# Kernel tuning notes

Hardware: AMD Instinct MI355X
Metric: run time of the kernel (lower is better)

## Reference

```python
import jax, jax.numpy as jnp
import numpy as np

B, S, D, H = 4, 1024, 256, 8  # batch, seq, d_model (== head_dim), n_heads
SCALE = 1.0 / float(np.sqrt(D))  # source references undefined self.scale; use 1/sqrt(d_model)


def setup_inputs() -> dict:
    key = jax.random.key(0)
    ks = jax.random.split(key, 11)
    w = 0.02
    return {
        "value_input": jax.random.normal(ks[0], (B, S, D), dtype=jnp.float32),
        "key_input": jax.random.normal(ks[1], (B, S, D), dtype=jnp.float32),
        "query_input": jax.random.normal(ks[2], (B, S, D), dtype=jnp.float32),
        "Wv": jax.random.normal(ks[3], (D, D * H), dtype=jnp.float32) * w,
        "bv": jnp.zeros((D * H,), dtype=jnp.float32),
        "Wk": jax.random.normal(ks[4], (D, D * H), dtype=jnp.float32) * w,
        "bk": jnp.zeros((D * H,), dtype=jnp.float32),
        "Wq": jax.random.normal(ks[5], (D, D * H), dtype=jnp.float32) * w,
        "bq": jnp.zeros((D * H,), dtype=jnp.float32),
        "Wo": jax.random.normal(ks[6], (D * H, D), dtype=jnp.float32) * w,
        "bo": jnp.zeros((D,), dtype=jnp.float32),
    }


def reference(value_input, key_input, query_input, Wv, bv, Wk, bk, Wq, bq, Wo, bo):
    # Fused QKV-style projections, then split into heads along last dim.
    # torch.split(..., d_model, dim=-1) == reshape to (B, S, H, D).
    v = (value_input @ Wv + bv).reshape(B, S, H, D)
    k = (key_input @ Wk + bk).reshape(B, S, H, D)
    q = (query_input @ Wq + bq).reshape(B, S, H, D)
    # Source: dot = k @ q^T  -> scores[b,h,key_pos,query_pos]
    scores = jnp.einsum('bkhd,bqhd->bhkq', k, q) * SCALE
    # Softmax over dim=-1 == the QUERY axis (faithful to source, nonstandard).
    attn = jax.nn.softmax(scores, axis=-1)
    # attn @ v : contract query axis with v's seq axis -> output indexed by key pos
    out_h = jnp.einsum('bhkq,bqhd->bkhd', attn, v)
    concat = out_h.reshape(B, S, H * D)
    return concat @ Wo + bo
```

## Files before the change

### kernel.cpp

```cpp
#include <hip/hip_runtime.h>
#include <cstddef>
#include <cstdint>

#define Bz 4
#define Sz 1024
#define Dm 256
#define Hh 8
#define DHh 2048
#define SCALE 0.0625f

typedef __attribute__((ext_vector_type(8))) short short8;
typedef __attribute__((ext_vector_type(16))) float f32x16;

__device__ inline unsigned short f2bf(float f){
  unsigned u = __float_as_uint(f);
  u += 0x7FFFu + ((u >> 16) & 1u);
  return (unsigned short)(u >> 16);
}
__device__ inline unsigned pk2(float a, float b){
  return (unsigned)f2bf(a) | ((unsigned)f2bf(b) << 16);
}
__device__ inline void gll16(const void* g, void* l){
  __builtin_amdgcn_global_load_lds((const __attribute__((address_space(1))) unsigned*)g,
                                   (__attribute__((address_space(3))) unsigned*)l, 16, 0, 0);
}
__device__ inline short8 lds8(const char* p){ return *(const short8*)p; }
__device__ inline f32x16 MM(short8 a, short8 b, f32x16 c){
  return __builtin_amdgcn_mfma_f32_32x32x16_bf16(a, b, c, 0, 0, 0);
}
__device__ inline f32x16 z16(){ f32x16 v;
#pragma unroll
  for(int i=0;i<16;i++) v[i]=0.f; return v; }

__global__ __launch_bounds__(256) void cvt_all(
    const float* __restrict__ S0, const float* __restrict__ S1, const float* __restrict__ S2,
    unsigned short* __restrict__ D0, unsigned short* __restrict__ D1, unsigned short* __restrict__ D2,
    const float* __restrict__ W0, const float* __restrict__ W1,
    const float* __restrict__ W2, const float* __restrict__ W3,
    unsigned short* __restrict__ T0, unsigned short* __restrict__ T1,
    unsigned short* __restrict__ T2, unsigned short* __restrict__ T3){
  __shared__ float t[32][33];
  int bx = blockIdx.x;
  if(bx < 3072){
    const int seg = bx >> 10;
    const float* src = seg==0 ? S0 : seg==1 ? S1 : S2;
    unsigned short* dst = seg==0 ? D0 : seg==1 ? D1 : D2;
    const int i = (bx & 1023)*256 + threadIdx.x;
    float4 v = ((const float4*)src)[i];
    ushort4 o; o.x=f2bf(v.x); o.y=f2bf(v.y); o.z=f2bf(v.z); o.w=f2bf(v.w);
    ((ushort4*)dst)[i] = o;
    return;
  }
  bx -= 3072;
  const int z = bx >> 9, inner = bx & 511;
  const float* W = z==0 ? W0 : z==1 ? W1 : z==2 ? W2 : W3;
  unsigned short* T = z==0 ? T0 : z==1 ? T1 : z==2 ? T2 : T3;
  const int K = (z<3) ? 256 : 2048;
  const int N = (z<3) ? 2048 : 256;
  const int n0 = (z<3) ? (inner & 63)*32 : (inner & 7)*32;
  const int k0 = (z<3) ? (inner >> 6)*32 : (inner >> 3)*32;
  const int a = threadIdx.x >> 5, c = threadIdx.x & 31;
#pragma unroll
  for(int p=0;p<4;p++)
    t[a + p*8][c] = W[(size_t)(k0 + a + p*8)*N + n0 + c];
  __syncthreads();
#pragma unroll
  for(int p=0;p<4;p++)
    T[(size_t)(n0 + a + p*8)*K + k0 + c] = f2bf(t[c][a + p*8]);
}

__global__ __launch_bounds__(256) void gemm_proj_all(
    const unsigned short* __restrict__ A0, const unsigned short* __restrict__ A1,
    const unsigned short* __restrict__ A2,
    const unsigned short* __restrict__ B0, const unsigned short* __restrict__ B1,
    const unsigned short* __restrict__ B2,
    const float* __restrict__ bias0, const float* __restrict__ bias1,
    const float* __restrict__ bias2,
    unsigned short* __restrict__ C0, unsigned short* __restrict__ C1,
    unsigned short* __restrict__ C2){
  __shared__ __align__(16) char sm[65536];
  const int z = blockIdx.z;
  const unsigned short* A = z==0 ? A0 : z==1 ? A1 : A2;
  const unsigned short* Bt = z==0 ? B0 : z==1 ? B1 : B2;
  const float* bias = z==0 ? bias0 : z==1 ? bias1 : bias2;
  unsigned short* C = z==0 ? C0 : z==1 ? C1 : C2;
  const int tid = threadIdx.x, w = tid>>6, lane = tid&63, l31 = lane&31, hp = lane>>5;
  const int wm = (w>>1)*64, wn = (w&1)*64;
  const int bm = blockIdx.y*128, bn = blockIdx.x*128;
  f32x16 acc[2][2]; acc[0][0]=z16(); acc[0][1]=z16(); acc[1][0]=z16(); acc[1][1]=z16();

  auto STAGE = [&](int db, int kk){
#pragma unroll
    for(int j=0;j<4;j++){
      int ci = (w*4+j)*64 + lane;
      int m = ci>>3, sl = ci&7;
      gll16(A  + (size_t)(bm+m)*256 + kk + ((sl ^ (m&7))<<3), sm + db*32768 + (w*4+j)*1024);
      gll16(Bt + (size_t)(bn+m)*256 + kk + ((sl ^ (m&7))<<3), sm + db*32768 + 16384 + (w*4+j)*1024);
    }
  };

  STAGE(0, 0);
  __syncthreads();
  int db = 0;
  for(int t=0; t<4; ++t){
    if(t<3) STAGE(db^1, (t+1)*64);
    const char* base = sm + db*32768;
#pragma unroll
    for(int s=0;s<4;s++){
      int m0 = wm + l31, m1 = wm + 32 + l31;
      int n0 = wn + l31, n1 = wn + 32 + l31;
      short8 a0 = lds8(base + m0*128 + (((s*2+hp) ^ (m0&7))<<4));
      short8 a1 = lds8(base + m1*128 + (((s*2+hp) ^ (m1&7))<<4));
      short8 b0 = lds8(base + 16384 + n0*128 + (((s*2+hp) ^ (n0&7))<<4));
      short8 b1 = lds8(base + 16384 + n1*128 + (((s*2+hp) ^ (n1&7))<<4));
      acc[0][0] = MM(a0,b0,acc[0][0]); acc[0][1] = MM(a0,b1,acc[0][1]);
      acc[1][0] = MM(a1,b0,acc[1][0]); acc[1][1] = MM(a1,b1,acc[1][1]);
    }
    __syncthreads();
    db ^= 1;
  }
#pragma unroll
  for(int nh=0; nh<2; nh++){
    int ncol = bn + wn + nh*32 + l31;
    float bb = bias[ncol];
#pragma unroll
    for(int mh=0; mh<2; mh++){
      if(z == 0){
        int hidx = ncol >> 8, d = ncol & 255;
#pragma unroll
        for(int gq=0; gq<4; gq++){
          int mrow = bm + wm + mh*32 + 8*gq + 4*hp;
          int batch = mrow >> 10, sin = mrow & 1023;
          int sblk = sin >> 3;
          unsigned u0 = pk2(acc[mh][nh][4*gq+0] + bb, acc[mh][nh][4*gq+1] + bb);
          unsigned u1 = pk2(acc[mh][nh][4*gq+2] + bb, acc[mh][nh][4*gq+3] + bb);
          uint2 uu; uu.x = u0; uu.y = u1;
          *(uint2*)(C + ((size_t)((batch*Hh + hidx)*128 + sblk)*256 + d)*8 + 4*hp) = uu;
        }
      } else {
        float sc = (z == 1) ? SCALE : 1.0f;
#pragma unroll
        for(int r=0; r<16; r++){
          int mrow = bm + wm + mh*32 + (r&3) + 8*(r>>2) + 4*hp;
          C[(size_t)mrow*DHh + ncol] = f2bf((acc[mh][nh][r] + bb) * sc);
        }
      }
    }
  }
}

__global__ __launch_bounds__(512, 2) void attn_mfma(
    const unsigned short* __restrict__ Kp, const unsigned short* __restrict__ Qp,
    const unsigned short* __restrict__ Vt, unsigned short* __restrict__ Oc){
  __shared__ __align__(16) char sm[67584];
  const int tid = threadIdx.x, w = tid>>6, lane = tid&63, l31 = lane&31, hp = lane>>5;
  const int set = w>>2, ws = w&3;
  const int bid = blockIdx.x;
  const int g = (bid & 7)*4 + (bid >> 6);
  const int b = g >> 3, h = g & 7;
  const int brow0 = ((bid >> 3) & 7) * 128;
  const size_t vtbase = (size_t)(b*Hh + h) * (Sz*Dm);

  short8 kp[16];
  {
    const unsigned short* kr = Kp + (size_t)(b*Sz + brow0 + ws*32 + l31)*DHh + h*Dm + hp*8;
#pragma unroll
    for(int ki=0; ki<16; ki++) kp[ki] = *(const short8*)(kr + ki*16);
  }
  f32x16 acc[8];
#pragma unroll
  for(int f=0; f<8; f++) acc[f] = z16();
  float m_run = -3.0e38f, l_run = 0.f;

  auto STAGE = [&](int db, int it){
    const int kv0 = set*512 + it*32;
    char* qpD = sm + db*32768 + set*16384;
#pragma unroll
    for(int j=0; j<4; j++){
      int slot = ws*4 + j;
      int ci = slot*64 + lane;
      int c = ci>>5, sl5 = ci&31;
      gll16(Qp + (size_t)(b*Sz + kv0 + c)*DHh + h*Dm + ((sl5 ^ c)<<3),
            qpD + slot*1024);
    }
  };

  STAGE(0, 0);
  __syncthreads();
  int db = 0;
  for(int it=0; it<16; ++it){
    if(it<15) STAGE(db^1, it+1);
    const char* qpL = sm + db*32768 + set*16384;
    f32x16 S = z16();
    __builtin_amdgcn_s_setprio(1);
#pragma unroll
    for(int ki=0; ki<16; ki++){
      short8 a = lds8(qpL + l31*512 + (((ki*2+hp) ^ l31)<<4));
      S = MM(a, kp[ki], S);
    }
    __builtin_amdgcn_s_setprio(0);
    float tmax = S[0];
#pragma unroll
    for(int r=1; r<16; r++) tmax = fmaxf(tmax, S[r]);
    tmax = fmaxf(tmax, __shfl_xor(tmax, 32));
    if(!__all(tmax <= m_run + 8.0f)){
      float mnew = fmaxf(m_run, tmax);
      float alpha = __expf(m_run - mnew);
      m_run = mnew; l_run *= alpha;
#pragma unroll
      for(int r=0; r<16; r++){
        int rr = (r&3) + 8*(r>>2) + 4*hp;
        float ar = __shfl(alpha, rr);
#pragma unroll
        for(int f=0; f<8; f++) acc[f][r] *= ar;
      }
    }
    float lsum = 0.f;
#pragma unroll
    for(int r=0; r<16; r++){ S[r] = __expf(S[r] - m_run); lsum += S[r]; }
    lsum += __shfl_xor(lsum, 32);
    l_run += lsum;
    short8 pa[2];
#pragma unroll
    for(int t=0; t<2; t++){
      unsigned w01 = pk2(S[t*8+0], S[t*8+1]);
      unsigned w23 = pk2(S[t*8+2], S[t*8+3]);
      unsigned w45 = pk2(S[t*8+4], S[t*8+5]);
      unsigned w67 = pk2(S[t*8+6], S[t*8+7]);
      unsigned x01 = __shfl_xor(w01, 32), x23 = __shfl_xor(w23, 32);
      unsigned x45 = __shfl_xor(w45, 32), x67 = __shfl_xor(w67, 32);
      union { unsigned u[4]; short8 s8; } U;
      if(hp == 0){ U.u[0]=w01; U.u[1]=w23; U.u[2]=x01; U.u[3]=x23; }
      else       { U.u[0]=x45; U.u[1]=x67; U.u[2]=w45; U.u[3]=w67; }
      pa[t] = U.s8;
    }
    const int sb0 = set*64 + it*4;
#pragma unroll
    for(int t=0; t<2; t++){
      const unsigned short* vrow = Vt + vtbase + (size_t)(sb0 + t*2 + hp)*2048;
      short8 vf[8];
#pragma unroll
      for(int f=0; f<8; f++)
        vf[f] = *(const short8*)(vrow + (f*32 + l31)*8);
      __builtin_amdgcn_s_setprio(1);
#pragma unroll
      for(int f=0; f<8; f++) acc[f] = MM(pa[t], vf[f], acc[f]);
      __builtin_amdgcn_s_setprio(0);
    }
    __syncthreads();
    db ^= 1;
  }
  __syncthreads();
  float* stats = (float*)(sm + 65536);
  if(lane < 32){ stats[(w*32 + lane)*2 + 0] = m_run; stats[(w*32 + lane)*2 + 1] = l_run; }
#pragma unroll
  for(int p=0; p<2; p++){
    __syncthreads();
    if(set == 1 && (ws>>1) == p){
      float mA = stats[(ws*32 + l31)*2 + 0];
      float mf = fmaxf(mA, m_run);
      float bB = __expf(m_run - mf);
      float* mg = (float*)sm + (ws&1)*8192;
#pragma unroll
      for(int r=0; r<16; r++){
        int rr = (r&3) + 8*(r>>2) + 4*hp;
        float br = __shfl(bB, rr);
#pragma unroll
        for(int f=0; f<8; f++) mg[rr*256 + f*32 + l31] = acc[f][r]*br;
      }
    }
    __syncthreads();
    if(set == 0 && (ws>>1) == p){
      float mB = stats[((4+ws)*32 + l31)*2 + 0];
      float lB = stats[((4+ws)*32 + l31)*2 + 1];
      float mf = fmaxf(m_run, mB);
      float bA = __expf(m_run - mf), bBv = __expf(mB - mf);
      float inv = 1.0f / (l_run*bA + lB*bBv);
      float* mg = (float*)sm + (ws&1)*8192;
#pragma unroll
      for(int r=0; r<16; r++){
        int rr = (r&3) + 8*(r>>2) + 4*hp;
        float bAr = __shfl(bA, rr);
        float invr = __shfl(inv, rr);
        int srow = brow0 + ws*32 + rr;
#pragma unroll
        for(int f=0; f<8; f++){
          float v = (acc[f][r]*bAr + mg[rr*256 + f*32 + l31]) * invr;
          Oc[(size_t)(b*Sz + srow)*DHh + h*Dm + f*32 + l31] = f2bf(v);
        }
      }
    }
  }
}

__global__ __launch_bounds__(256) void gemm_out(const unsigned short* __restrict__ A,
    const unsigned short* __restrict__ Bt, const float* __restrict__ bias,
    float* __restrict__ C){
  __shared__ __align__(16) char sm[32768];
  const int tid = threadIdx.x, w = tid>>6, lane = tid&63, l31 = lane&31, hp = lane>>5;
  const int wm = (w>>1)*32, wn = (w&1)*32;
  const int bm = blockIdx.y*64, bn = blockIdx.x*64;
  f32x16 acc = z16();

  auto STAGE = [&](int db, int kk){
#pragma unroll
    for(int j=0; j<2; j++){
      int ci = (w*2+j)*64 + lane;
      int m = ci>>3, sl = ci&7;
      gll16(A  + (size_t)(bm+m)*DHh + kk + ((sl ^ (m&7))<<3), sm + db*16384 + (w*2+j)*1024);
      gll16(Bt + (size_t)(bn+m)*DHh + kk + ((sl ^ (m&7))<<3), sm + db*16384 + 8192 + (w*2+j)*1024);
    }
  };

  STAGE(0, 0);
  __syncthreads();
  int db = 0;
  for(int t=0; t<32; ++t){
    if(t<31) STAGE(db^1, (t+1)*64);
    const char* base = sm + db*16384;
#pragma unroll
    for(int s=0; s<4; s++){
      int m0 = wm + l31, n0 = wn + l31;
      short8 a = lds8(base + m0*128 + (((s*2+hp) ^ (m0&7))<<4));
      short8 b = lds8(base + 8192 + n0*128 + (((s*2+hp) ^ (n0&7))<<4));
      acc = MM(a, b, acc);
    }
    __syncthreads();
    db ^= 1;
  }
  float bb = bias[bn + wn + l31];
#pragma unroll
  for(int r=0; r<16; r++){
    int mrow = bm + wm + (r&3) + 8*(r>>2) + 4*hp;
    C[(size_t)mrow*Dm + bn + wn + l31] = acc[r] + bb;
  }
}

extern "C" void kernel_launch(void* const* d_in, const int* in_sizes, int n_in,
                              void* d_out, int out_size, void* d_ws, size_t ws_size,
                              hipStream_t stream){
  (void)in_sizes; (void)n_in; (void)out_size; (void)ws_size;
  const float* value_in = (const float*)d_in[0];
  const float* key_in   = (const float*)d_in[1];
  const float* query_in = (const float*)d_in[2];
  const float* Wv = (const float*)d_in[3];
  const float* bv = (const float*)d_in[4];
  const float* Wk = (const float*)d_in[5];
  const float* bk = (const float*)d_in[6];
  const float* Wq = (const float*)d_in[7];
  const float* bq = (const float*)d_in[8];
  const float* Wo = (const float*)d_in[9];
  const float* bo = (const float*)d_in[10];

  char* ws = (char*)d_ws;
  unsigned short* av  = (unsigned short*)(ws + ((size_t) 0u<<20));
  unsigned short* ak  = (unsigned short*)(ws + ((size_t) 2u<<20));
  unsigned short* aq  = (unsigned short*)(ws + ((size_t) 4u<<20));
  unsigned short* wtv = (unsigned short*)(ws + ((size_t) 6u<<20));
  unsigned short* wtk = (unsigned short*)(ws + ((size_t) 7u<<20));
  unsigned short* wtq = (unsigned short*)(ws + ((size_t) 8u<<20));
  unsigned short* wto = (unsigned short*)(ws + ((size_t) 9u<<20));
  unsigned short* vt  = (unsigned short*)(ws + ((size_t)10u<<20));
  unsigned short* kb  = (unsigned short*)(ws + ((size_t)26u<<20));
  unsigned short* qb  = (unsigned short*)(ws + ((size_t)42u<<20));
  unsigned short* cc  = (unsigned short*)(ws + ((size_t)58u<<20));

  cvt_all<<<5120, 256, 0, stream>>>(value_in, key_in, query_in, av, ak, aq,
                                    Wv, Wk, Wq, Wo, wtv, wtk, wtq, wto);

  gemm_proj_all<<<dim3(16, 32, 3), 256, 0, stream>>>(
      av, ak, aq, wtv, wtk, wtq, bv, bk, bq, vt, kb, qb);

  attn_mfma<<<256, 512, 0, stream>>>(kb, qb, vt, cc);

  gemm_out<<<dim3(4, 64), 256, 0, stream>>>(cc, wto, bo, (float*)d_out);
}
```

Before: 209.8 us.

## Halve attention block row tile to 64 rows and launch 512 four-wave blocks

The attention kernel now processes 64 key rows per block with 4 waves (2 row groups × 2 KV-halves) instead of 128 rows with 8 waves, doubling the grid to 512 blocks. The block-to-(batch, head, row) mapping is rewritten to keep XCD grouping, each wave issues twice as many Q staging loads, and the two-pass merge of the KV-split partial results becomes a single pass. The aim is better load balance and more resident blocks per CU. The cost is that each staged Q tile is reused across half as many rows, so global/L2 traffic for Q roughly doubles.

```diff
diff --git a/kernel.cpp b/kernel.cpp
--- a/kernel.cpp
+++ b/kernel.cpp
@@ -149,21 +149,22 @@
   }
 }
 
-__global__ __launch_bounds__(512, 2) void attn_mfma(
+__global__ __launch_bounds__(256, 2) void attn_mfma(
     const unsigned short* __restrict__ Kp, const unsigned short* __restrict__ Qp,
     const unsigned short* __restrict__ Vt, unsigned short* __restrict__ Oc){
-  __shared__ __align__(16) char sm[67584];
+  __shared__ __align__(16) char sm[66560];
   const int tid = threadIdx.x, w = tid>>6, lane = tid&63, l31 = lane&31, hp = lane>>5;
-  const int set = w>>2, ws = w&3;
+  const int rg = w&1, set = w>>1;
   const int bid = blockIdx.x;
-  const int g = (bid & 7)*4 + (bid >> 6);
-  const int b = g >> 3, h = g & 7;
-  const int brow0 = ((bid >> 3) & 7) * 128;
+  const int xcd = bid & 7, inner = bid >> 3;
+  const int rb = inner & 15, gsub = inner >> 4;
+  const int g = gsub*8 + xcd, b = g >> 3, h = g & 7;
+  const int brow0 = rb * 64;
   const size_t vtbase = (size_t)(b*Hh + h) * (Sz*Dm);
 
   short8 kp[16];
   {
-    const unsigned short* kr = Kp + (size_t)(b*Sz + brow0 + ws*32 + l31)*DHh + h*Dm + hp*8;
+    const unsigned short* kr = Kp + (size_t)(b*Sz + brow0 + rg*32 + l31)*DHh + h*Dm + hp*8;
 #pragma unroll
     for(int ki=0; ki<16; ki++) kp[ki] = *(const short8*)(kr + ki*16);
   }
@@ -176,8 +177,8 @@
     const int kv0 = set*512 + it*32;
     char* qpD = sm + db*32768 + set*16384;
 #pragma unroll
-    for(int j=0; j<4; j++){
-      int slot = ws*4 + j;
+    for(int j=0; j<8; j++){
+      int slot = rg*8 + j;
       int ci = slot*64 + lane;
       int c = ci>>5, sl5 = ci&31;
       gll16(Qp + (size_t)(b*Sz + kv0 + c)*DHh + h*Dm + ((sl5 ^ c)<<3),
@@ -253,41 +254,37 @@
   __syncthreads();
   float* stats = (float*)(sm + 65536);
   if(lane < 32){ stats[(w*32 + lane)*2 + 0] = m_run; stats[(w*32 + lane)*2 + 1] = l_run; }
-#pragma unroll
-  for(int p=0; p<2; p++){
-    __syncthreads();
-    if(set == 1 && (ws>>1) == p){
-      float mA = stats[(ws*32 + l31)*2 + 0];
-      float mf = fmaxf(mA, m_run);
-      float bB = __expf(m_run - mf);
-      float* mg = (float*)sm + (ws&1)*8192;
-#pragma unroll
-      for(int r=0; r<16; r++){
-        int rr = (r&3) + 8*(r>>2) + 4*hp;
-        float br = __shfl(bB, rr);
-#pragma unroll
-        for(int f=0; f<8; f++) mg[rr*256 + f*32 + l31] = acc[f][r]*br;
-      }
-    }
-    __syncthreads();
-    if(set == 0 && (ws>>1) == p){
-      float mB = stats[((4+ws)*32 + l31)*2 + 0];
-      float lB = stats[((4+ws)*32 + l31)*2 + 1];
-      float mf = fmaxf(m_run, mB);
-      float bA = __expf(m_run - mf), bBv = __expf(mB - mf);
-      float inv = 1.0f / (l_run*bA + lB*bBv);
-      float* mg = (float*)sm + (ws&1)*8192;
-#pragma unroll
-      for(int r=0; r<16; r++){
-        int rr = (r&3) + 8*(r>>2) + 4*hp;
-        float bAr = __shfl(bA, rr);
-        float invr = __shfl(inv, rr);
-        int srow = brow0 + ws*32 + rr;
-#pragma unroll
-        for(int f=0; f<8; f++){
-          float v = (acc[f][r]*bAr + mg[rr*256 + f*32 + l31]) * invr;
-          Oc[(size_t)(b*Sz + srow)*DHh + h*Dm + f*32 + l31] = f2bf(v);
-        }
+  __syncthreads();
+  float* mg = (float*)sm + rg*8192;
+  if(set == 1){
+    float mA = stats[(rg*32 + l31)*2 + 0];
+    float mf = fmaxf(mA, m_run);
+    float bB = __expf(m_run - mf);
+#pragma unroll
+    for(int r=0; r<16; r++){
+      int rr = (r&3) + 8*(r>>2) + 4*hp;
+      float br = __shfl(bB, rr);
+#pragma unroll
+      for(int f=0; f<8; f++) mg[rr*256 + f*32 + l31] = acc[f][r]*br;
+    }
+  }
+  __syncthreads();
+  if(set == 0){
+    float mB = stats[((2+rg)*32 + l31)*2 + 0];
+    float lB = stats[((2+rg)*32 + l31)*2 + 1];
+    float mf = fmaxf(m_run, mB);
+    float bA = __expf(m_run - mf), bBv = __expf(mB - mf);
+    float inv = 1.0f / (l_run*bA + lB*bBv);
+#pragma unroll
+    for(int r=0; r<16; r++){
+      int rr = (r&3) + 8*(r>>2) + 4*hp;
+      float bAr = __shfl(bA, rr);
+      float invr = __shfl(inv, rr);
+      int srow = brow0 + rg*32 + rr;
+#pragma unroll
+      for(int f=0; f<8; f++){
+        float v = (acc[f][r]*bAr + mg[rr*256 + f*32 + l31]) * invr;
+        Oc[(size_t)(b*Sz + srow)*DHh + h*Dm + f*32 + l31] = f2bf(v);
       }
     }
   }
@@ -371,7 +368,7 @@
   gemm_proj_all<<<dim3(16, 32, 3), 256, 0, stream>>>(
       av, ak, aq, wtv, wtk, wtq, bv, bk, bq, vt, kb, qb);
 
-  attn_mfma<<<256, 512, 0, stream>>>(kb, qb, vt, cc);
+  attn_mfma<<<512, 256, 0, stream>>>(kb, qb, vt, cc);
 
   gemm_out<<<dim3(4, 64), 256, 0, stream>>>(cc, wto, bo, (float*)d_out);
 }
```

After: 214.3 us. 2.2% more time.
